# Kernel tuning notes

Measured on AMD Instinct MI355X. Metric: run time of the kernel, lower is better.

Reference implementation:

```python
import jax, jax.numpy as jnp
import numpy as np

EX = 100.0
EY = 100.0
EXPONENT = 3.8
ZUSER = 0.0
ZAP = 1.0
NUSER = 256          # = Nap
NAP = 256
NUD = 10 * NUSER     # Nuser_drop = 2560
BATCH = 32           # batch_num
B2 = 2 * BATCH       # internal doubled batch
LN10 = jnp.log(10.0)


def _toroidal_dist(Xap, Xuser):
    # Xap: [B2, Nap, 3], Xuser: [B2, Nud, 3] -> D: [B2, Nap, Nud]
    dx = jnp.abs(Xap[:, :, None, 0] - Xuser[:, None, :, 0])
    dx = jnp.minimum(dx, EX - dx)
    dy = jnp.abs(Xap[:, :, None, 1] - Xuser[:, None, :, 1])
    dy = jnp.minimum(dy, EY - dy)
    dz = Xap[:, :, None, 2] - Xuser[:, None, :, 2]
    return jnp.sqrt(dx * dx + dy * dy + dz * dz)


def setup_inputs() -> dict:
    key = jax.random.key(0)
    k1, k2 = jax.random.split(key)
    xy_ap = jax.random.uniform(k1, (B2, NAP, 2), dtype=jnp.float32) * EX
    xy_us = jax.random.uniform(k2, (B2, NUD, 2), dtype=jnp.float32) * EX
    Xap = jnp.concatenate([xy_ap, jnp.full((B2, NAP, 1), ZAP, jnp.float32)], axis=2)
    Xuser = jnp.concatenate([xy_us, jnp.full((B2, NUD, 1), ZUSER, jnp.float32)], axis=2)
    return {"Xap": Xap, "Xuser": Xuser, "batch_num": BATCH}


def reference(Xap, Xuser, batch_num):
    D = _toroidal_dist(Xap, Xuser)                      # [B2, Nap, Nud]
    d_sort = jnp.argmin(D, axis=1)                      # [B2, Nud] nearest AP per user
    # indicator[b, i, j] = 1 if user j is assigned to AP i
    ind = (d_sort[:, None, :] == jnp.arange(NAP)[None, :, None])
    mask = jnp.arange(1.0, NUD + 1.0, dtype=jnp.float32)  # [Nud]
    mask_i = mask[None, None, :] * ind.astype(jnp.float32)  # [B2, Nap, Nud]
    # softmax-round trick from Assign_AP: one-hot at the max-index assigned user
    onehot = jnp.round(jax.nn.softmax(100.0 * mask_i, axis=-1))
    # D_assign[b, a, i] = distance from AP a to the user selected for AP i
    D_assign = jnp.einsum('bij,baj->bai', onehot, D)[:batch_num]  # [B, Nap, Nuser]
    g = -46.0 - 10.0 * EXPONENT * jnp.log(D_assign) / LN10
    g_linear = jnp.power(10.0, g / 10.0)                # G: [B, Nap, Nuser]
    # beta_open_loop = 1 (default)
    power_propotional = 1.0 / jnp.diagonal(g_linear, axis1=1, axis2=2)  # [B, Nap]
    return g_linear, power_propotional
```

## Files before the change

### kernel.cpp

```cpp
#include <hip/hip_runtime.h>
#include <math.h>

#define NAP   256
#define NUD   2560
#define BATCH 32
#define EXT   100.0f

__global__ void init_sel_kernel(int* __restrict__ sel) {
    sel[blockIdx.x * blockDim.x + threadIdx.x] = -1;
}

__global__ __launch_bounds__(256) void assign_kernel(
    const float* __restrict__ Xap, const float* __restrict__ Xuser,
    int* __restrict__ sel)
{
    const int b = blockIdx.y;
    const int t = threadIdx.x;
    const int c = t & 3;
    const int j = blockIdx.x * 64 + (t >> 2);

    __shared__ float sx[4 * 65], sy[4 * 65], sz[4 * 65];
    {
        const float* ap = Xap + ((size_t)b * NAP + t) * 3;
        const int idx = (t >> 6) * 65 + (t & 63);
        sx[idx] = ap[0]; sy[idx] = ap[1]; sz[idx] = ap[2];
    }
    __syncthreads();

    const float* up = Xuser + ((size_t)b * NUD + j) * 3;
    const float ux = up[0], uy = up[1], uz = up[2];

    float best = INFINITY;
    int besta = 0;
    const int base = c * 65;
    #pragma unroll 8
    for (int k = 0; k < 64; ++k) {
        float dx = fabsf(sx[base + k] - ux); dx = fminf(dx, EXT - dx);
        float dy = fabsf(sy[base + k] - uy); dy = fminf(dy, EXT - dy);
        float dz = sz[base + k] - uz;
        float d  = sqrtf(dx * dx + dy * dy + dz * dz);
        if (d < best) { best = d; besta = c * 64 + k; }
    }
    #pragma unroll
    for (int off = 1; off <= 2; off <<= 1) {
        const float d_o = __shfl_xor(best, off);
        const int   a_o = __shfl_xor(besta, off);
        if (d_o < best || (d_o == best && a_o < besta)) { best = d_o; besta = a_o; }
    }
    if (c == 0) atomicMax(&sel[b * NAP + besta], j);
}

__global__ __launch_bounds__(256) void gain_kernel(
    const float* __restrict__ Xap, const float* __restrict__ Xuser,
    const int* __restrict__ sel, float* __restrict__ out)
{
    const int b = blockIdx.y;
    const int a = blockIdx.x;
    const int i = threadIdx.x;

    const int j = sel[b * NAP + i];

    float gl = 0.0f;
    float pw = 0.0f;
    if (j >= 0) {
        const float* up  = Xuser + ((size_t)b * NUD + j) * 3;
        const float* app = Xap   + ((size_t)b * NAP + a) * 3;
        float dx = fabsf(app[0] - up[0]); dx = fminf(dx, EXT - dx);
        float dy = fabsf(app[1] - up[1]); dy = fminf(dy, EXT - dy);
        float dz = app[2] - up[2];
        float D  = sqrtf(dx * dx + dy * dy + dz * dz);
        const float g = -46.0f - 38.0f * (logf(D) * 0.43429448190325176f);
        gl = exp10f(g * 0.1f);
        pw = 1.0f / gl;
    }

    out[((size_t)b * NAP + a) * NAP + i] = gl;
    if (i == a) {
        out[(size_t)BATCH * NAP * NAP + (size_t)b * NAP + a] = pw;
    }
}

extern "C" void kernel_launch(void* const* d_in, const int* in_sizes, int n_in,
                              void* d_out, int out_size, void* d_ws, size_t ws_size,
                              hipStream_t stream) {
    const float* Xap   = (const float*)d_in[0];
    const float* Xuser = (const float*)d_in[1];
    int*   sel = (int*)d_ws;
    float* out = (float*)d_out;

    hipLaunchKernelGGL(init_sel_kernel, dim3(BATCH), dim3(NAP), 0, stream, sel);
    hipLaunchKernelGGL(assign_kernel, dim3(NUD / 64, BATCH), dim3(256), 0, stream,
                       Xap, Xuser, sel);
    hipLaunchKernelGGL(gain_kernel, dim3(NAP, BATCH), dim3(NAP), 0, stream,
                       Xap, Xuser, sel, out);
}
```

Baseline: 85.97 us.

## Drop init kernel, move per-AP selection into shared-memory atomics in gain kernel

The nearest-AP kernel now writes each user's nearest AP index to workspace instead of doing global atomicMax. The gain kernel rebuilds the per-AP selection in shared memory with LDS atomics, which removes the separate init launch. Each block now handles 8 APs, so user coordinates are loaded once and reused across them. The cost is that every gain block redundantly scans all 2560 nearest indices for its batch, 32 times per batch, and the grid shrinks to 1024 blocks.

```diff
diff --git a/kernel.cpp b/kernel.cpp
--- a/kernel.cpp
+++ b/kernel.cpp
@@ -5,14 +5,11 @@
 #define NUD   2560
 #define BATCH 32
 #define EXT   100.0f
+#define ATILE 8
 
-__global__ void init_sel_kernel(int* __restrict__ sel) {
-    sel[blockIdx.x * blockDim.x + threadIdx.x] = -1;
-}
-
-__global__ __launch_bounds__(256) void assign_kernel(
+__global__ __launch_bounds__(256) void nearest_kernel(
     const float* __restrict__ Xap, const float* __restrict__ Xuser,
-    int* __restrict__ sel)
+    int* __restrict__ nearest)
 {
     const int b = blockIdx.y;
     const int t = threadIdx.x;
@@ -47,36 +44,59 @@
         const int   a_o = __shfl_xor(besta, off);
         if (d_o < best || (d_o == best && a_o < besta)) { best = d_o; besta = a_o; }
     }
-    if (c == 0) atomicMax(&sel[b * NAP + besta], j);
+    if (c == 0) nearest[b * NUD + j] = besta;
 }
 
 __global__ __launch_bounds__(256) void gain_kernel(
     const float* __restrict__ Xap, const float* __restrict__ Xuser,
-    const int* __restrict__ sel, float* __restrict__ out)
+    const int* __restrict__ nearest, float* __restrict__ out)
 {
     const int b = blockIdx.y;
-    const int a = blockIdx.x;
+    const int g = blockIdx.x;
     const int i = threadIdx.x;
 
-    const int j = sel[b * NAP + i];
+    __shared__ int   sel[NAP];
+    __shared__ float apx[ATILE], apy[ATILE], apz[ATILE];
 
-    float gl = 0.0f;
-    float pw = 0.0f;
+    sel[i] = -1;
+    if (i < ATILE) {
+        const float* ap = Xap + ((size_t)b * NAP + g * ATILE + i) * 3;
+        apx[i] = ap[0]; apy[i] = ap[1]; apz[i] = ap[2];
+    }
+    __syncthreads();
+
+    const int* nb = nearest + b * NUD;
+    #pragma unroll
+    for (int r = 0; r < NUD / NAP; ++r) {
+        const int j = r * NAP + i;
+        atomicMax(&sel[nb[j]], j);
+    }
+    __syncthreads();
+
+    const int j = sel[i];
+    float ux = 0.0f, uy = 0.0f, uz = 0.0f;
     if (j >= 0) {
-        const float* up  = Xuser + ((size_t)b * NUD + j) * 3;
-        const float* app = Xap   + ((size_t)b * NAP + a) * 3;
-        float dx = fabsf(app[0] - up[0]); dx = fminf(dx, EXT - dx);
-        float dy = fabsf(app[1] - up[1]); dy = fminf(dy, EXT - dy);
-        float dz = app[2] - up[2];
-        float D  = sqrtf(dx * dx + dy * dy + dz * dz);
-        const float g = -46.0f - 38.0f * (logf(D) * 0.43429448190325176f);
-        gl = exp10f(g * 0.1f);
-        pw = 1.0f / gl;
+        const float* up = Xuser + ((size_t)b * NUD + j) * 3;
+        ux = up[0]; uy = up[1]; uz = up[2];
     }
 
-    out[((size_t)b * NAP + a) * NAP + i] = gl;
-    if (i == a) {
-        out[(size_t)BATCH * NAP * NAP + (size_t)b * NAP + a] = pw;
+    #pragma unroll
+    for (int k = 0; k < ATILE; ++k) {
+        const int a = g * ATILE + k;
+        float gl = 0.0f, pw = 0.0f;
+        if (j >= 0) {
+            float dx = fabsf(apx[k] - ux); dx = fminf(dx, EXT - dx);
+            float dy = fabsf(apy[k] - uy); dy = fminf(dy, EXT - dy);
+            float dz = apz[k] - uz;
+            float D  = sqrtf(dx * dx + dy * dy + dz * dz);
+            const float gg = -46.0f - 38.0f * (logf(D) * 0.43429448190325176f);
+            gl = exp10f(gg * 0.1f);
+            pw = 1.0f / gl;
+        }
+        out[((size_t)b * NAP + a) * NAP + i] = gl;
+        if (i == a) {
+            out[(size_t)BATCH * NAP * NAP + (size_t)b * NAP + a] = pw;
+        }
     }
 }
 
@@ -85,12 +105,11 @@
                               hipStream_t stream) {
     const float* Xap   = (const float*)d_in[0];
     const float* Xuser = (const float*)d_in[1];
-    int*   sel = (int*)d_ws;
-    float* out = (float*)d_out;
+    int*   nearest = (int*)d_ws;
+    float* out     = (float*)d_out;
 
-    hipLaunchKernelGGL(init_sel_kernel, dim3(BATCH), dim3(NAP), 0, stream, sel);
-    hipLaunchKernelGGL(assign_kernel, dim3(NUD / 64, BATCH), dim3(256), 0, stream,
-                       Xap, Xuser, sel);
-    hipLaunchKernelGGL(gain_kernel, dim3(NAP, BATCH), dim3(NAP), 0, stream,
-                       Xap, Xuser, sel, out);
+    hipLaunchKernelGGL(nearest_kernel, dim3(NUD / 64, BATCH), dim3(256), 0, stream,
+                       Xap, Xuser, nearest);
+    hipLaunchKernelGGL(gain_kernel, dim3(NAP / ATILE, BATCH), dim3(256), 0, stream,
+                       Xap, Xuser, nearest, out);
 }
```

Measured after the change: 83.64 us. 1.03x faster.
